# Performance work log

Hardware: AMD Instinct MI355X
Metric: run time of the kernel (lower is better)

## Reference

```python
import jax, jax.numpy as jnp
import numpy as np

BS, D, C, L_MAP, N_LAYERS, IMG = 8, 512, 128, 8, 9, 64


def _leaky(x):
    return jnp.where(x >= 0, x, 0.2 * x)


def _conv2d_mod(x, style, weight):
    # x: [bs, C, H, W], style: [bs, C], weight: [Cout, Cin, 3, 3]
    # modulate along input-channel dim, demodulate per (sample, out-channel)
    mw = weight[None] * style[:, None, :, None, None]          # [bs, Cout, Cin, 3, 3]
    rstd = jax.lax.rsqrt(jnp.sum(mw * mw, axis=(2, 3, 4), keepdims=True) + 1e-8)
    dw = mw * rstd                                             # demodulated per-sample weights

    def per_sample(xi, wi):
        return jax.lax.conv_general_dilated(
            xi[None], wi, window_strides=(1, 1), padding='SAME',
            dimension_numbers=('NCHW', 'OIHW', 'NCHW'))[0]

    return jax.vmap(per_sample)(x, dw)                         # [bs, C, H, W]


def _upsample2x(x):
    b, c, h, w = x.shape
    return jax.image.resize(x, (b, c, 2 * h, 2 * w), method='bilinear')


def setup_inputs():
    key = jax.random.key(0)
    ks = jax.random.split(key, 10)
    # kaiming fan_in gain for leaky_relu(a=0) per nn.init in Conv2dMod
    conv_std = float(np.sqrt(2.0 / (C * 9)))
    return {
        'latent_z': jax.random.normal(ks[0], (BS, D), jnp.float32),
        'noise': jax.random.normal(ks[1], (N_LAYERS, BS, IMG * IMG), jnp.float32),
        'map_w': jax.random.normal(ks[2], (L_MAP, D, D), jnp.float32) / np.sqrt(D),
        'map_b': jnp.zeros((L_MAP, D), jnp.float32),
        'A_w': jax.random.normal(ks[3], (N_LAYERS, D, C), jnp.float32) / np.sqrt(D),
        'A_b': jax.random.normal(ks[4], (N_LAYERS, C), jnp.float32) * 0.02 + 1.0,
        'B_w': jax.random.normal(ks[5], (N_LAYERS, C), jnp.float32),
        'B_b': jax.random.normal(ks[6], (N_LAYERS, C), jnp.float32) * 0.02,
        'conv_w': jax.random.normal(ks[7], (N_LAYERS, C, C, 3, 3), jnp.float32) * conv_std,
        'rgb_w': jax.random.normal(ks[8], (3, C, 3, 3), jnp.float32) / np.sqrt(C * 9),
        'rgb_b': jnp.zeros((3,), jnp.float32),
    }


def reference(latent_z, noise, map_w, map_b, A_w, A_b, B_w, B_b, conv_w, rgb_w, rgb_b):
    # ---- Mapping: PixelNorm + n_map_layers FC+LeakyReLU ----
    w = latent_z * jax.lax.rsqrt(jnp.mean(latent_z * latent_z, axis=1, keepdims=True) + 1e-8)
    for i in range(L_MAP):
        w = _leaky(w @ map_w[i] + map_b[i])                    # [bs, D] (same w for every style layer)

    # ---- Synthesis ----
    x = jnp.zeros((BS, C, 4, 4), latent_z.dtype)
    for i in range(N_LAYERS):
        if i % 2 == 1:
            x = _upsample2x(x)
        b, c, h, wd = x.shape
        ns = h * wd
        style = w @ A_w[i] + A_b[i]                            # [bs, C]
        # B: Linear(1, C) on per-pixel noise scalar -> per-channel noise map
        nmap = noise[i][:, :ns, None] * B_w[i][None, None, :] + B_b[i]  # [bs, ns, C]
        nmap = jnp.transpose(nmap, (0, 2, 1)).reshape(b, C, h, wd)
        x = _leaky(_conv2d_mod(x, style, conv_w[i]) + nmap)

    # ---- to RGB ----
    rgb = jax.lax.conv_general_dilated(
        x, rgb_w, window_strides=(1, 1), padding='SAME',
        dimension_numbers=('NCHW', 'OIHW', 'NCHW')) + rgb_b[None, :, None, None]
    return rgb
```

## Files before the change

### kernel.cpp

```cpp
#include <hip/hip_runtime.h>
#include <hip/hip_bf16.h>

#define BS 8
#define D 512
#define CCH 128
#define LMAP 8
#define NLAYERS 9

typedef short short8 __attribute__((ext_vector_type(8)));
typedef short short4v __attribute__((ext_vector_type(4)));
typedef float f32x4 __attribute__((ext_vector_type(4)));

__device__ short g_bufA[(size_t)BS * 4096 * CCH];
__device__ short g_bufB[(size_t)BS * 4096 * CCH];
__device__ float g_w[2][BS * D];
__device__ float g_style_all[NLAYERS * BS * CCH];
__device__ float g_rstd_all[NLAYERS * BS * CCH];
__device__ short g_wpack[(size_t)NLAYERS * 9 * 4 * 8 * 64 * 8];
__device__ short g_rgbpack[9 * 4 * 64 * 8];

__device__ __forceinline__ float leaky(float v) { return v >= 0.f ? v : 0.2f * v; }
__device__ __forceinline__ short f2b(float f) {
    __hip_bfloat16 h = __float2bfloat16(f);
    return *reinterpret_cast<short*>(&h);
}
__device__ __forceinline__ float b2f(short s) {
    return __uint_as_float(((unsigned int)(unsigned short)s) << 16);
}
__device__ __forceinline__ int swz(int col) { return ((col ^ (col >> 3)) & 7) << 3; }

__device__ __forceinline__ void uptaps(int o, int Win, int& i0, int& i1, float& w0, float& w1)
{
    int m = o >> 1;
    if ((o & 1) == 0) { i0 = m - 1; i1 = m; w0 = 0.25f; w1 = 0.75f; if (i0 < 0) { i0 = 0; w0 = 0.f; w1 = 1.f; } }
    else              { i0 = m; i1 = m + 1; w0 = 0.75f; w1 = 0.25f; if (i1 >= Win) { i1 = Win - 1; w0 = 1.f; w1 = 0.f; } }
}

__global__ __launch_bounds__(256) void wprep_kernel(const float* __restrict__ convw)
{
    int idx = blockIdx.x * 256 + threadIdx.x;
    if (idx >= NLAYERS * 9 * 4 * 8 * 64) return;
    int lane = idx & 63;
    int cogrp = (idx >> 6) & 7;
    int chunk = (idx >> 9) & 3;
    int t = idx >> 11;
    int layer = t / 9, tap = t - layer * 9;
    int co = cogrp * 16 + (lane & 15);
    int ci0 = chunk * 32 + (lane >> 4) * 8;
    short8 v;
#pragma unroll
    for (int j = 0; j < 8; ++j)
        v[j] = f2b(convw[(((size_t)layer * CCH + co) * CCH + ci0 + j) * 9 + tap]);
    *reinterpret_cast<short8*>(&g_wpack[(size_t)idx * 8]) = v;
}

__global__ void rgbprep_kernel(const float* __restrict__ rgbw)
{
    int idx = blockIdx.x * 256 + threadIdx.x;
    if (idx >= 9 * 4 * 64) return;
    int lane = idx & 63;
    int chunk = (idx >> 6) & 3;
    int tap = idx >> 8;
    int co = lane & 15;
    int ci0 = chunk * 32 + (lane >> 4) * 8;
    short8 v;
#pragma unroll
    for (int j = 0; j < 8; ++j)
        v[j] = (co < 3) ? f2b(rgbw[((size_t)(co * CCH) + ci0 + j) * 9 + tap]) : (short)0;
    *reinterpret_cast<short8*>(&g_rgbpack[(size_t)idx * 8]) = v;
}

__global__ __launch_bounds__(256) void map_fc_kernel(
    int srcSel, int useZ, const float* __restrict__ z,
    const float* __restrict__ W, const float* __restrict__ bias)
{
    float* wout = g_w[srcSel ^ 1];
    int b = blockIdx.y;
    int jb = blockIdx.x * 64;
    int tid = threadIdx.x;
    int jl = tid & 63, kp = tid >> 6;
    __shared__ float xin[D];
    __shared__ float part[4][64];
    __shared__ float wred[4];
    if (useZ) {
        xin[tid] = z[b * D + tid];
        xin[tid + 256] = z[b * D + tid + 256];
    } else {
        const float* win = g_w[srcSel];
        xin[tid] = win[b * D + tid];
        xin[tid + 256] = win[b * D + tid + 256];
    }
    __syncthreads();
    if (useZ) {
        float p = xin[tid] * xin[tid] + xin[tid + 256] * xin[tid + 256];
#pragma unroll
        for (int off = 32; off > 0; off >>= 1) p += __shfl_down(p, off, 64);
        if ((tid & 63) == 0) wred[tid >> 6] = p;
        __syncthreads();
        float ss = wred[0] + wred[1] + wred[2] + wred[3];
        float r = rsqrtf(ss * (1.f / 512.f) + 1e-8f);
        xin[tid] *= r; xin[tid + 256] *= r;
        __syncthreads();
    }
    const float* Wp = W + jb + jl;
    const int k0 = kp * 128;
    float a0 = 0.f, a1 = 0.f, a2 = 0.f, a3 = 0.f, a4 = 0.f, a5 = 0.f, a6 = 0.f, a7 = 0.f;
    for (int k = k0; k < k0 + 128; k += 8) {
        a0 += xin[k + 0] * Wp[(size_t)(k + 0) * D];
        a1 += xin[k + 1] * Wp[(size_t)(k + 1) * D];
        a2 += xin[k + 2] * Wp[(size_t)(k + 2) * D];
        a3 += xin[k + 3] * Wp[(size_t)(k + 3) * D];
        a4 += xin[k + 4] * Wp[(size_t)(k + 4) * D];
        a5 += xin[k + 5] * Wp[(size_t)(k + 5) * D];
        a6 += xin[k + 6] * Wp[(size_t)(k + 6) * D];
        a7 += xin[k + 7] * Wp[(size_t)(k + 7) * D];
    }
    part[kp][jl] = ((a0 + a1) + (a2 + a3)) + ((a4 + a5) + (a6 + a7));
    __syncthreads();
    if (tid < 64) {
        float s = part[0][tid] + part[1][tid] + part[2][tid] + part[3][tid] + bias[jb + tid];
        wout[b * D + jb + tid] = leaky(s);
    }
}

__global__ __launch_bounds__(256) void style_rstd_kernel(
    const float* __restrict__ Aw, const float* __restrict__ Ab,
    const float* __restrict__ convw)
{
    int l = blockIdx.x + 1;
    int b = blockIdx.y;
    int tid = threadIdx.x;
    __shared__ float ws_[D];
    __shared__ float part[2][CCH];
    __shared__ float st[CCH];
    ws_[tid] = g_w[0][b * D + tid];
    ws_[tid + 256] = g_w[0][b * D + tid + 256];
    __syncthreads();
    {
        int c = tid & 127, kh = tid >> 7;
        const float* Ap = Aw + (size_t)l * D * CCH + c;
        const int k0 = kh * 256;
        float a0 = 0.f, a1 = 0.f, a2 = 0.f, a3 = 0.f, a4 = 0.f, a5 = 0.f, a6 = 0.f, a7 = 0.f;
        for (int k = k0; k < k0 + 256; k += 8) {
            a0 += ws_[k + 0] * Ap[(size_t)(k + 0) * CCH];
            a1 += ws_[k + 1] * Ap[(size_t)(k + 1) * CCH];
            a2 += ws_[k + 2] * Ap[(size_t)(k + 2) * CCH];
            a3 += ws_[k + 3] * Ap[(size_t)(k + 3) * CCH];
            a4 += ws_[k + 4] * Ap[(size_t)(k + 4) * CCH];
            a5 += ws_[k + 5] * Ap[(size_t)(k + 5) * CCH];
            a6 += ws_[k + 6] * Ap[(size_t)(k + 6) * CCH];
            a7 += ws_[k + 7] * Ap[(size_t)(k + 7) * CCH];
        }
        part[kh][c] = ((a0 + a1) + (a2 + a3)) + ((a4 + a5) + (a6 + a7));
    }
    __syncthreads();
    if (tid < CCH) {
        float s = part[0][tid] + part[1][tid] + Ab[l * CCH + tid];
        st[tid] = s;
        g_style_all[((size_t)l * BS + b) * CCH + tid] = s;
    }
    __syncthreads();
    int colid = tid >> 4, kpart = tid & 15;
    for (int co8 = 0; co8 < 8; ++co8) {
        int cout = co8 * 16 + colid;
        const float* wp = convw + ((size_t)(l * CCH + cout) * CCH + kpart * 8) * 9;
        float wf[72];
#pragma unroll
        for (int q = 0; q < 18; ++q) {
            float4 t = *reinterpret_cast<const float4*>(wp + q * 4);
            wf[q * 4 + 0] = t.x; wf[q * 4 + 1] = t.y; wf[q * 4 + 2] = t.z; wf[q * 4 + 3] = t.w;
        }
        float s = 0.f;
#pragma unroll
        for (int ci = 0; ci < 8; ++ci) {
            float sv = st[kpart * 8 + ci];
#pragma unroll
            for (int k = 0; k < 9; ++k) { float m = wf[ci * 9 + k] * sv; s += m * m; }
        }
#pragma unroll
        for (int off = 8; off > 0; off >>= 1) s += __shfl_down(s, off, 16);
        if (kpart == 0) g_rstd_all[((size_t)l * BS + b) * CCH + cout] = rsqrtf(s + 1e-8f);
    }
}

template<int LW, int UPM>
__global__ __launch_bounds__(256) void conv_mfma_kernel(
    int srcSel, int layer, int layerNext,
    const float* __restrict__ noise,
    const float* __restrict__ Bw, const float* __restrict__ Bb,
    const float* __restrict__ noise0,
    const float* __restrict__ Bw0, const float* __restrict__ Bb0)
{
    constexpr int W = 1 << LW;
    constexpr int R = 64 >> LW;
    constexpr int SW = W + 2;
    constexpr int ROWS = R + 2;
    constexpr int NS = W * W;
    constexpr int WIN = W / 2;

    const short* xin = srcSel ? g_bufB : g_bufA;
    short* xout = srcSel ? g_bufA : g_bufB;

    const int b = blockIdx.y;
    const int pixBase = blockIdx.x * 64;
    const int rowBase = pixBase >> LW;
    const int tid = threadIdx.x;
    const int lane = tid & 63;
    const int wave = tid >> 6;
    const int wpx = wave & 1;
    const int wco = wave >> 1;

    __shared__ short xs[ROWS * SW * CCH];
    __shared__ float style_s[CCH];
    constexpr int SMSZ = (UPM == 2) ? 16 * CCH : 1;
    __shared__ short sm[SMSZ];

    if (tid < CCH)
        style_s[tid] = layerNext ? g_style_all[((size_t)layerNext * BS + b) * CCH + tid] : 1.f;

    if (UPM == 2) {
        for (int u = tid; u < 16 * CCH; u += 256) {
            int c = u & 127;
            int pp = u >> 7;
            float v = leaky(noise0[b * 4096 + pp] * Bw0[c] + Bb0[c])
                      * g_style_all[((size_t)1 * BS + b) * CCH + c];
            sm[u] = f2b(v);
        }
        __syncthreads();
    }

    {
        const short* src = xin + (size_t)b * NS * CCH;
        const short* srcH = xin + (size_t)b * WIN * WIN * CCH;
        constexpr int UN = ROWS * SW * 16;
        for (int u = tid; u < UN; u += 256) {
            int ck = u & 15;
            int rem = u >> 4;
            int col = rem % SW;
            int rr = rem / SW;
            int gy = rowBase + rr - 1, gx = col - 1;
            short8 v = {0, 0, 0, 0, 0, 0, 0, 0};
            if (gy >= 0 && gy < W && gx >= 0 && gx < W) {
                if (UPM == 0) {
                    v = *reinterpret_cast<const short8*>(&src[((size_t)gy * W + gx) * CCH + ck * 8]);
                } else {
                    int y0, y1, x0, x1; float wy0, wy1, wx0, wx1;
                    uptaps(gy, WIN, y0, y1, wy0, wy1);
                    uptaps(gx, WIN, x0, x1, wx0, wx1);
                    const short* sp = (UPM == 2) ? sm : srcH;
                    short8 a00 = *reinterpret_cast<const short8*>(&sp[((size_t)y0 * WIN + x0) * CCH + ck * 8]);
                    short8 a01 = *reinterpret_cast<const short8*>(&sp[((size_t)y0 * WIN + x1) * CCH + ck * 8]);
                    short8 a10 = *reinterpret_cast<const short8*>(&sp[((size_t)y1 * WIN + x0) * CCH + ck * 8]);
                    short8 a11 = *reinterpret_cast<const short8*>(&sp[((size_t)y1 * WIN + x1) * CCH + ck * 8]);
                    float w00 = wy0 * wx0, w01 = wy0 * wx1, w10 = wy1 * wx0, w11 = wy1 * wx1;
#pragma unroll
                    for (int j = 0; j < 8; ++j)
                        v[j] = f2b(w00 * b2f(a00[j]) + w01 * b2f(a01[j])
                                 + w10 * b2f(a10[j]) + w11 * b2f(a11[j]));
                }
            }
            *reinterpret_cast<short8*>(&xs[(((rr * SW + col) * CCH) + ck * 8) ^ swz(col)]) = v;
        }
    }
    __syncthreads();

    int rL[2], cL[2];
#pragma unroll
    for (int pf = 0; pf < 2; ++pf) {
        int pl = (wpx * 2 + pf) * 16 + (lane & 15);
        cL[pf] = pl & (W - 1);
        rL[pf] = pl >> LW;
    }
    const int grpoff = (lane >> 4) * 8;

    f32x4 acc[2][4] = {};
    const short* wl = g_wpack + ((size_t)layer * 9 * 4 * 8 * 64
                                 + (size_t)(wco * 4) * 64 + lane) * 8;

    short8 wc0 = *reinterpret_cast<const short8*>(wl);
    short8 wc1 = *reinterpret_cast<const short8*>(wl + 512);
    short8 wc2 = *reinterpret_cast<const short8*>(wl + 1024);
    short8 wc3 = *reinterpret_cast<const short8*>(wl + 1536);
#pragma unroll
    for (int k = 0; k < 36; ++k) {
        short8 wn0 = wc0, wn1 = wc1, wn2 = wc2, wn3 = wc3;
        if (k + 1 < 36) {
            const short* wk = wl + (size_t)(k + 1) * 4096;
            wn0 = *reinterpret_cast<const short8*>(wk);
            wn1 = *reinterpret_cast<const short8*>(wk + 512);
            wn2 = *reinterpret_cast<const short8*>(wk + 1024);
            wn3 = *reinterpret_cast<const short8*>(wk + 1536);
        }
        const int tap = k >> 2, ch = k & 3;
        const int ky = tap / 3, kx = tap - ky * 3;
#pragma unroll
        for (int pf = 0; pf < 2; ++pf) {
            int col = cL[pf] + kx;
            int idx = (((rL[pf] + ky) * SW + col) * CCH + (ch << 5) + grpoff) ^ swz(col);
            short8 xf = *reinterpret_cast<const short8*>(&xs[idx]);
            acc[pf][0] = __builtin_amdgcn_mfma_f32_16x16x32_bf16(wc0, xf, acc[pf][0], 0, 0, 0);
            acc[pf][1] = __builtin_amdgcn_mfma_f32_16x16x32_bf16(wc1, xf, acc[pf][1], 0, 0, 0);
            acc[pf][2] = __builtin_amdgcn_mfma_f32_16x16x32_bf16(wc2, xf, acc[pf][2], 0, 0, 0);
            acc[pf][3] = __builtin_amdgcn_mfma_f32_16x16x32_bf16(wc3, xf, acc[pf][3], 0, 0, 0);
        }
        wc0 = wn0; wc1 = wn1; wc2 = wn2; wc3 = wn3;
    }

    float nz[2];
#pragma unroll
    for (int pf = 0; pf < 2; ++pf)
        nz[pf] = noise[b * 4096 + pixBase + (wpx * 2 + pf) * 16 + (lane & 15)];
#pragma unroll
    for (int cf = 0; cf < 4; ++cf) {
        const int coB = (wco * 4 + cf) * 16 + (lane >> 4) * 4;
        float rs[4], bw[4], bb[4], sn[4];
#pragma unroll
        for (int r = 0; r < 4; ++r) {
            rs[r] = g_rstd_all[((size_t)layer * BS + b) * CCH + coB + r];
            bw[r] = Bw[coB + r];
            bb[r] = Bb[coB + r];
            sn[r] = style_s[coB + r];
        }
#pragma unroll
        for (int pf = 0; pf < 2; ++pf) {
            int px = pixBase + (wpx * 2 + pf) * 16 + (lane & 15);
            short4v o;
#pragma unroll
            for (int r = 0; r < 4; ++r) {
                float v = leaky(acc[pf][cf][r] * rs[r] + nz[pf] * bw[r] + bb[r]) * sn[r];
                o[r] = f2b(v);
            }
            *reinterpret_cast<short4v*>(&xout[((size_t)b * NS + px) * CCH + coB]) = o;
        }
    }
}

__global__ __launch_bounds__(256) void rgb_mfma_kernel(
    int srcSel, const float* __restrict__ rgbb, float* __restrict__ out)
{
    constexpr int W = 64, SW = 66, ROWS = 3, NS = 4096;
    const short* xin = srcSel ? g_bufB : g_bufA;

    const int b = blockIdx.y;
    const int pixBase = blockIdx.x * 64;
    const int rowBase = pixBase >> 6;
    const int tid = threadIdx.x;
    const int lane = tid & 63;
    const int wave = tid >> 6;

    __shared__ short xs[ROWS * SW * CCH];

    {
        const short* src = xin + (size_t)b * NS * CCH;
        constexpr int UN = ROWS * SW * 16;
        for (int u = tid; u < UN; u += 256) {
            int ck = u & 15;
            int rem = u >> 4;
            int col = rem % SW;
            int rr = rem / SW;
            int gy = rowBase + rr - 1, gx = col - 1;
            short8 v = {0, 0, 0, 0, 0, 0, 0, 0};
            if (gy >= 0 && gy < W && gx >= 0 && gx < W)
                v = *reinterpret_cast<const short8*>(&src[((size_t)gy * W + gx) * CCH + ck * 8]);
            *reinterpret_cast<short8*>(&xs[(((rr * SW + col) * CCH) + ck * 8) ^ swz(col)]) = v;
        }
    }
    __syncthreads();

    const int grpoff = (lane >> 4) * 8;
    const int cl = lane & 15;
    f32x4 acc[4] = {};
#pragma unroll
    for (int tap = 0; tap < 9; ++tap) {
        const int ky = tap / 3, kx = tap - ky * 3;
        short8 wf = *reinterpret_cast<const short8*>(
            &g_rgbpack[((size_t)(tap * 4 + wave) * 64 + lane) * 8]);
#pragma unroll
        for (int pf = 0; pf < 4; ++pf) {
            int col = cl + pf * 16 + kx;
            int idx = ((ky * SW + col) * CCH + (wave << 5) + grpoff) ^ swz(col);
            short8 xf = *reinterpret_cast<const short8*>(&xs[idx]);
            acc[pf] = __builtin_amdgcn_mfma_f32_16x16x32_bf16(wf, xf, acc[pf], 0, 0, 0);
        }
    }
    __syncthreads();
    float* red = reinterpret_cast<float*>(xs);
    if (wave > 0) {
#pragma unroll
        for (int pf = 0; pf < 4; ++pf)
#pragma unroll
            for (int r = 0; r < 4; ++r)
                red[(((wave - 1) * 4 + pf) * 64 + lane) * 4 + r] = acc[pf][r];
    }
    __syncthreads();
    if (wave == 0 && (lane >> 4) == 0) {
#pragma unroll
        for (int pf = 0; pf < 4; ++pf) {
            int px = pixBase + pf * 16 + cl;
#pragma unroll
            for (int r = 0; r < 3; ++r) {
                float s = acc[pf][r];
#pragma unroll
                for (int wv = 0; wv < 3; ++wv)
                    s += red[((wv * 4 + pf) * 64 + lane) * 4 + r];
                out[(size_t)(b * 3 + r) * NS + px] = s + rgbb[r];
            }
        }
    }
}

extern "C" void kernel_launch(void* const* d_in, const int* in_sizes, int n_in,
                              void* d_out, int out_size, void* d_ws, size_t ws_size,
                              hipStream_t stream)
{
    const float* latent = (const float*)d_in[0];
    const float* noise  = (const float*)d_in[1];
    const float* map_w  = (const float*)d_in[2];
    const float* map_b  = (const float*)d_in[3];
    const float* A_w    = (const float*)d_in[4];
    const float* A_b    = (const float*)d_in[5];
    const float* B_w    = (const float*)d_in[6];
    const float* B_b    = (const float*)d_in[7];
    const float* conv_w = (const float*)d_in[8];
    const float* rgb_w  = (const float*)d_in[9];
    const float* rgb_b  = (const float*)d_in[10];
    float* out = (float*)d_out;
    (void)d_ws; (void)ws_size;

    wprep_kernel<<<(NLAYERS * 9 * 4 * 8 * 64 + 255) / 256, 256, 0, stream>>>(conv_w);
    rgbprep_kernel<<<(9 * 4 * 64 + 255) / 256, 256, 0, stream>>>(rgb_w);

    int wsel = 0;
    for (int i = 0; i < LMAP; ++i) {
        map_fc_kernel<<<dim3(8, BS), 256, 0, stream>>>(
            wsel, i == 0 ? 1 : 0, latent, map_w + (size_t)i * D * D, map_b + i * D);
        wsel ^= 1;
    }

    style_rstd_kernel<<<dim3(8, BS), 256, 0, stream>>>(A_w, A_b, conv_w);

    int cur = 1;
    int Hc = 4;
    for (int i = 1; i < NLAYERS; ++i) {
        if (i & 1) Hc *= 2;
        int ns = Hc * Hc;
        int lnext = (i < 8) ? (i + 1) : 0;
        dim3 grid(ns / 64, BS);
        const float* nz = noise + (size_t)i * BS * 4096;
        switch (i) {
            case 1: conv_mfma_kernel<3, 2><<<grid, 256, 0, stream>>>(cur, i, lnext, nz, B_w + i * CCH, B_b + i * CCH, noise, B_w, B_b); break;
            case 2: conv_mfma_kernel<3, 0><<<grid, 256, 0, stream>>>(cur, i, lnext, nz, B_w + i * CCH, B_b + i * CCH, noise, B_w, B_b); break;
            case 3: conv_mfma_kernel<4, 1><<<grid, 256, 0, stream>>>(cur, i, lnext, nz, B_w + i * CCH, B_b + i * CCH, noise, B_w, B_b); break;
            case 4: conv_mfma_kernel<4, 0><<<grid, 256, 0, stream>>>(cur, i, lnext, nz, B_w + i * CCH, B_b + i * CCH, noise, B_w, B_b); break;
            case 5: conv_mfma_kernel<5, 1><<<grid, 256, 0, stream>>>(cur, i, lnext, nz, B_w + i * CCH, B_b + i * CCH, noise, B_w, B_b); break;
            case 6: conv_mfma_kernel<5, 0><<<grid, 256, 0, stream>>>(cur, i, lnext, nz, B_w + i * CCH, B_b + i * CCH, noise, B_w, B_b); break;
            case 7: conv_mfma_kernel<6, 1><<<grid, 256, 0, stream>>>(cur, i, lnext, nz, B_w + i * CCH, B_b + i * CCH, noise, B_w, B_b); break;
            case 8: conv_mfma_kernel<6, 0><<<grid, 256, 0, stream>>>(cur, i, lnext, nz, B_w + i * CCH, B_b + i * CCH, noise, B_w, B_b); break;
        }
        cur ^= 1;
    }

    rgb_mfma_kernel<<<dim3(64, BS), 256, 0, stream>>>(cur, rgb_b, out);
}
```

Baseline: 229.3 us.

## Fuse prep kernels, precompute weight sum-of-squares, fuse 8x8 conv layer pair

Merges the weight-pack and rgb-pack prep kernels into one launch. That launch also precomputes per-(cout,cin) sums of squared 3x3 weights, so the demodulation rstd becomes a cheap style-squared dot product. Layers 1 and 2 at 8x8 run in a single per-sample kernel that keeps the intermediate activation in shared memory, which removes one launch and a global round trip. The map FC loop is widened to 16 accumulators. The fused conv pair launches only 8 blocks, so its GPU utilisation is low.

```diff
diff --git a/kernel.cpp b/kernel.cpp
--- a/kernel.cpp
+++ b/kernel.cpp
@@ -16,6 +16,7 @@
 __device__ float g_w[2][BS * D];
 __device__ float g_style_all[NLAYERS * BS * CCH];
 __device__ float g_rstd_all[NLAYERS * BS * CCH];
+__device__ float g_s2[(size_t)NLAYERS * CCH * CCH];
 __device__ short g_wpack[(size_t)NLAYERS * 9 * 4 * 8 * 64 * 8];
 __device__ short g_rgbpack[9 * 4 * 64 * 8];
 
@@ -36,38 +37,46 @@
     else              { i0 = m; i1 = m + 1; w0 = 0.75f; w1 = 0.25f; if (i1 >= Win) { i1 = Win - 1; w0 = 1.f; w1 = 0.f; } }
 }
 
-__global__ __launch_bounds__(256) void wprep_kernel(const float* __restrict__ convw)
+#define WPN (NLAYERS * 9 * 4 * 8 * 64)
+#define RGBN (9 * 4 * 64)
+#define S2N (NLAYERS * CCH * CCH)
+__global__ __launch_bounds__(256) void prep_kernel(
+    const float* __restrict__ convw, const float* __restrict__ rgbw)
 {
     int idx = blockIdx.x * 256 + threadIdx.x;
-    if (idx >= NLAYERS * 9 * 4 * 8 * 64) return;
-    int lane = idx & 63;
-    int cogrp = (idx >> 6) & 7;
-    int chunk = (idx >> 9) & 3;
-    int t = idx >> 11;
-    int layer = t / 9, tap = t - layer * 9;
-    int co = cogrp * 16 + (lane & 15);
-    int ci0 = chunk * 32 + (lane >> 4) * 8;
-    short8 v;
-#pragma unroll
-    for (int j = 0; j < 8; ++j)
-        v[j] = f2b(convw[(((size_t)layer * CCH + co) * CCH + ci0 + j) * 9 + tap]);
-    *reinterpret_cast<short8*>(&g_wpack[(size_t)idx * 8]) = v;
-}
-
-__global__ void rgbprep_kernel(const float* __restrict__ rgbw)
-{
-    int idx = blockIdx.x * 256 + threadIdx.x;
-    if (idx >= 9 * 4 * 64) return;
-    int lane = idx & 63;
-    int chunk = (idx >> 6) & 3;
-    int tap = idx >> 8;
-    int co = lane & 15;
-    int ci0 = chunk * 32 + (lane >> 4) * 8;
-    short8 v;
-#pragma unroll
-    for (int j = 0; j < 8; ++j)
-        v[j] = (co < 3) ? f2b(rgbw[((size_t)(co * CCH) + ci0 + j) * 9 + tap]) : (short)0;
-    *reinterpret_cast<short8*>(&g_rgbpack[(size_t)idx * 8]) = v;
+    if (idx < WPN) {
+        int lane = idx & 63;
+        int cogrp = (idx >> 6) & 7;
+        int chunk = (idx >> 9) & 3;
+        int t = idx >> 11;
+        int layer = t / 9, tap = t - layer * 9;
+        int co = cogrp * 16 + (lane & 15);
+        int ci0 = chunk * 32 + (lane >> 4) * 8;
+        short8 v;
+#pragma unroll
+        for (int j = 0; j < 8; ++j)
+            v[j] = f2b(convw[(((size_t)layer * CCH + co) * CCH + ci0 + j) * 9 + tap]);
+        *reinterpret_cast<short8*>(&g_wpack[(size_t)idx * 8]) = v;
+    } else if (idx < WPN + RGBN) {
+        int u = idx - WPN;
+        int lane = u & 63;
+        int chunk = (u >> 6) & 3;
+        int tap = u >> 8;
+        int co = lane & 15;
+        int ci0 = chunk * 32 + (lane >> 4) * 8;
+        short8 v;
+#pragma unroll
+        for (int j = 0; j < 8; ++j)
+            v[j] = (co < 3) ? f2b(rgbw[((size_t)(co * CCH) + ci0 + j) * 9 + tap]) : (short)0;
+        *reinterpret_cast<short8*>(&g_rgbpack[(size_t)u * 8]) = v;
+    } else if (idx < WPN + RGBN + S2N) {
+        int u = idx - WPN - RGBN;
+        const float* wp = convw + (size_t)u * 9;
+        float s = 0.f;
+#pragma unroll
+        for (int t = 0; t < 9; ++t) { float m = wp[t]; s += m * m; }
+        g_s2[u] = s;
+    }
 }
 
 __global__ __launch_bounds__(256) void map_fc_kernel(
@@ -104,18 +113,18 @@
     }
     const float* Wp = W + jb + jl;
     const int k0 = kp * 128;
-    float a0 = 0.f, a1 = 0.f, a2 = 0.f, a3 = 0.f, a4 = 0.f, a5 = 0.f, a6 = 0.f, a7 = 0.f;
-    for (int k = k0; k < k0 + 128; k += 8) {
-        a0 += xin[k + 0] * Wp[(size_t)(k + 0) * D];
-        a1 += xin[k + 1] * Wp[(size_t)(k + 1) * D];
-        a2 += xin[k + 2] * Wp[(size_t)(k + 2) * D];
-        a3 += xin[k + 3] * Wp[(size_t)(k + 3) * D];
-        a4 += xin[k + 4] * Wp[(size_t)(k + 4) * D];
-        a5 += xin[k + 5] * Wp[(size_t)(k + 5) * D];
-        a6 += xin[k + 6] * Wp[(size_t)(k + 6) * D];
-        a7 += xin[k + 7] * Wp[(size_t)(k + 7) * D];
-    }
-    part[kp][jl] = ((a0 + a1) + (a2 + a3)) + ((a4 + a5) + (a6 + a7));
+    float a[16];
+#pragma unroll
+    for (int j = 0; j < 16; ++j) a[j] = 0.f;
+    for (int k = k0; k < k0 + 128; k += 16) {
+#pragma unroll
+        for (int j = 0; j < 16; ++j)
+            a[j] += xin[k + j] * Wp[(size_t)(k + j) * D];
+    }
+    float s8 = 0.f;
+#pragma unroll
+    for (int j = 0; j < 16; ++j) s8 += a[j];
+    part[kp][jl] = s8;
     __syncthreads();
     if (tid < 64) {
         float s = part[0][tid] + part[1][tid] + part[2][tid] + part[3][tid] + bias[jb + tid];
@@ -124,8 +133,7 @@
 }
 
 __global__ __launch_bounds__(256) void style_rstd_kernel(
-    const float* __restrict__ Aw, const float* __restrict__ Ab,
-    const float* __restrict__ convw)
+    const float* __restrict__ Aw, const float* __restrict__ Ab)
 {
     int l = blockIdx.x + 1;
     int b = blockIdx.y;
@@ -161,25 +169,209 @@
     }
     __syncthreads();
     int colid = tid >> 4, kpart = tid & 15;
+#pragma unroll
     for (int co8 = 0; co8 < 8; ++co8) {
         int cout = co8 * 16 + colid;
-        const float* wp = convw + ((size_t)(l * CCH + cout) * CCH + kpart * 8) * 9;
-        float wf[72];
-#pragma unroll
-        for (int q = 0; q < 18; ++q) {
-            float4 t = *reinterpret_cast<const float4*>(wp + q * 4);
-            wf[q * 4 + 0] = t.x; wf[q * 4 + 1] = t.y; wf[q * 4 + 2] = t.z; wf[q * 4 + 3] = t.w;
-        }
+        const float* sp = g_s2 + ((size_t)l * CCH + cout) * CCH + kpart * 8;
         float s = 0.f;
 #pragma unroll
-        for (int ci = 0; ci < 8; ++ci) {
-            float sv = st[kpart * 8 + ci];
-#pragma unroll
-            for (int k = 0; k < 9; ++k) { float m = wf[ci * 9 + k] * sv; s += m * m; }
-        }
+        for (int j = 0; j < 8; ++j) { float sv = st[kpart * 8 + j]; s += sv * sv * sp[j]; }
 #pragma unroll
         for (int off = 8; off > 0; off >>= 1) s += __shfl_down(s, off, 16);
         if (kpart == 0) g_rstd_all[((size_t)l * BS + b) * CCH + cout] = rsqrtf(s + 1e-8f);
+    }
+}
+
+__global__ __launch_bounds__(256) void conv8_pair_kernel(
+    const float* __restrict__ noise,
+    const float* __restrict__ Bw, const float* __restrict__ Bb)
+{
+    constexpr int W = 8, SW = 10, ROWS = 10, NS = 64, WIN = 4;
+    const int b = blockIdx.x;
+    const int tid = threadIdx.x;
+    const int lane = tid & 63;
+    const int wave = tid >> 6;
+    const int wpx = wave & 1;
+    const int wco = wave >> 1;
+
+    __shared__ short xs1[ROWS * SW * CCH];
+    __shared__ short xs2[ROWS * SW * CCH];
+    __shared__ short sm[16 * CCH];
+    __shared__ float style2_s[CCH], style3_s[CCH];
+
+    if (tid < CCH) {
+        style2_s[tid] = g_style_all[((size_t)2 * BS + b) * CCH + tid];
+        style3_s[tid] = g_style_all[((size_t)3 * BS + b) * CCH + tid];
+    }
+    for (int u = tid; u < 16 * CCH; u += 256) {
+        int c = u & 127;
+        int pp = u >> 7;
+        float v = leaky(noise[b * 4096 + pp] * Bw[c] + Bb[c])
+                  * g_style_all[((size_t)1 * BS + b) * CCH + c];
+        sm[u] = f2b(v);
+    }
+    for (int u = tid; u < ROWS * SW * 16; u += 256) {
+        int ck = u & 15;
+        int cell = u >> 4;
+        int col = cell % SW;
+        int rr = cell / SW;
+        if (rr >= 1 && rr <= 8 && col >= 1 && col <= 8) continue;
+        short8 z = {0, 0, 0, 0, 0, 0, 0, 0};
+        *reinterpret_cast<short8*>(&xs2[(((rr * SW + col) * CCH) + ck * 8) ^ swz(col)]) = z;
+    }
+    __syncthreads();
+
+    for (int u = tid; u < ROWS * SW * 16; u += 256) {
+        int ck = u & 15;
+        int rem = u >> 4;
+        int col = rem % SW;
+        int rr = rem / SW;
+        int gy = rr - 1, gx = col - 1;
+        short8 v = {0, 0, 0, 0, 0, 0, 0, 0};
+        if (gy >= 0 && gy < W && gx >= 0 && gx < W) {
+            int y0, y1, x0, x1; float wy0, wy1, wx0, wx1;
+            uptaps(gy, WIN, y0, y1, wy0, wy1);
+            uptaps(gx, WIN, x0, x1, wx0, wx1);
+            short8 a00 = *reinterpret_cast<const short8*>(&sm[((size_t)y0 * WIN + x0) * CCH + ck * 8]);
+            short8 a01 = *reinterpret_cast<const short8*>(&sm[((size_t)y0 * WIN + x1) * CCH + ck * 8]);
+            short8 a10 = *reinterpret_cast<const short8*>(&sm[((size_t)y1 * WIN + x0) * CCH + ck * 8]);
+            short8 a11 = *reinterpret_cast<const short8*>(&sm[((size_t)y1 * WIN + x1) * CCH + ck * 8]);
+            float w00 = wy0 * wx0, w01 = wy0 * wx1, w10 = wy1 * wx0, w11 = wy1 * wx1;
+#pragma unroll
+            for (int j = 0; j < 8; ++j)
+                v[j] = f2b(w00 * b2f(a00[j]) + w01 * b2f(a01[j])
+                         + w10 * b2f(a10[j]) + w11 * b2f(a11[j]));
+        }
+        *reinterpret_cast<short8*>(&xs1[(((rr * SW + col) * CCH) + ck * 8) ^ swz(col)]) = v;
+    }
+    __syncthreads();
+
+    int rL[2], cL[2];
+#pragma unroll
+    for (int pf = 0; pf < 2; ++pf) {
+        int pl = (wpx * 2 + pf) * 16 + (lane & 15);
+        cL[pf] = pl & (W - 1);
+        rL[pf] = pl >> 3;
+    }
+    const int grpoff = (lane >> 4) * 8;
+
+    {
+        f32x4 acc[2][4] = {};
+        const short* wl = g_wpack + ((size_t)1 * 9 * 4 * 8 * 64 + (size_t)(wco * 4) * 64 + lane) * 8;
+        short8 wc0 = *reinterpret_cast<const short8*>(wl);
+        short8 wc1 = *reinterpret_cast<const short8*>(wl + 512);
+        short8 wc2 = *reinterpret_cast<const short8*>(wl + 1024);
+        short8 wc3 = *reinterpret_cast<const short8*>(wl + 1536);
+#pragma unroll
+        for (int k = 0; k < 36; ++k) {
+            short8 wn0 = wc0, wn1 = wc1, wn2 = wc2, wn3 = wc3;
+            if (k + 1 < 36) {
+                const short* wk = wl + (size_t)(k + 1) * 4096;
+                wn0 = *reinterpret_cast<const short8*>(wk);
+                wn1 = *reinterpret_cast<const short8*>(wk + 512);
+                wn2 = *reinterpret_cast<const short8*>(wk + 1024);
+                wn3 = *reinterpret_cast<const short8*>(wk + 1536);
+            }
+            const int tap = k >> 2, ch = k & 3;
+            const int ky = tap / 3, kx = tap - ky * 3;
+#pragma unroll
+            for (int pf = 0; pf < 2; ++pf) {
+                int col = cL[pf] + kx;
+                int idx = (((rL[pf] + ky) * SW + col) * CCH + (ch << 5) + grpoff) ^ swz(col);
+                short8 xf = *reinterpret_cast<const short8*>(&xs1[idx]);
+                acc[pf][0] = __builtin_amdgcn_mfma_f32_16x16x32_bf16(wc0, xf, acc[pf][0], 0, 0, 0);
+                acc[pf][1] = __builtin_amdgcn_mfma_f32_16x16x32_bf16(wc1, xf, acc[pf][1], 0, 0, 0);
+                acc[pf][2] = __builtin_amdgcn_mfma_f32_16x16x32_bf16(wc2, xf, acc[pf][2], 0, 0, 0);
+                acc[pf][3] = __builtin_amdgcn_mfma_f32_16x16x32_bf16(wc3, xf, acc[pf][3], 0, 0, 0);
+            }
+            wc0 = wn0; wc1 = wn1; wc2 = wn2; wc3 = wn3;
+        }
+        float nz[2];
+#pragma unroll
+        for (int pf = 0; pf < 2; ++pf)
+            nz[pf] = noise[(size_t)BS * 4096 + b * 4096 + (wpx * 2 + pf) * 16 + (lane & 15)];
+#pragma unroll
+        for (int cf = 0; cf < 4; ++cf) {
+            const int coB = (wco * 4 + cf) * 16 + (lane >> 4) * 4;
+            float rs[4], bw[4], bb[4], sn[4];
+#pragma unroll
+            for (int r = 0; r < 4; ++r) {
+                rs[r] = g_rstd_all[((size_t)1 * BS + b) * CCH + coB + r];
+                bw[r] = Bw[1 * CCH + coB + r];
+                bb[r] = Bb[1 * CCH + coB + r];
+                sn[r] = style2_s[coB + r];
+            }
+#pragma unroll
+            for (int pf = 0; pf < 2; ++pf) {
+                int px = (wpx * 2 + pf) * 16 + (lane & 15);
+                int y = px >> 3, x = px & 7;
+                short4v o;
+#pragma unroll
+                for (int r = 0; r < 4; ++r)
+                    o[r] = f2b(leaky(acc[pf][cf][r] * rs[r] + nz[pf] * bw[r] + bb[r]) * sn[r]);
+                int col = x + 1;
+                *reinterpret_cast<short4v*>(&xs2[((((y + 1) * SW + col) * CCH) + coB) ^ swz(col)]) = o;
+            }
+        }
+    }
+    __syncthreads();
+
+    {
+        f32x4 acc[2][4] = {};
+        const short* wl = g_wpack + ((size_t)2 * 9 * 4 * 8 * 64 + (size_t)(wco * 4) * 64 + lane) * 8;
+        short8 wc0 = *reinterpret_cast<const short8*>(wl);
+        short8 wc1 = *reinterpret_cast<const short8*>(wl + 512);
+        short8 wc2 = *reinterpret_cast<const short8*>(wl + 1024);
+        short8 wc3 = *reinterpret_cast<const short8*>(wl + 1536);
+#pragma unroll
+        for (int k = 0; k < 36; ++k) {
+            short8 wn0 = wc0, wn1 = wc1, wn2 = wc2, wn3 = wc3;
+            if (k + 1 < 36) {
+                const short* wk = wl + (size_t)(k + 1) * 4096;
+                wn0 = *reinterpret_cast<const short8*>(wk);
+                wn1 = *reinterpret_cast<const short8*>(wk + 512);
+                wn2 = *reinterpret_cast<const short8*>(wk + 1024);
+                wn3 = *reinterpret_cast<const short8*>(wk + 1536);
+            }
+            const int tap = k >> 2, ch = k & 3;
+            const int ky = tap / 3, kx = tap - ky * 3;
+#pragma unroll
+            for (int pf = 0; pf < 2; ++pf) {
+                int col = cL[pf] + kx;
+                int idx = (((rL[pf] + ky) * SW + col) * CCH + (ch << 5) + grpoff) ^ swz(col);
+                short8 xf = *reinterpret_cast<const short8*>(&xs2[idx]);
+                acc[pf][0] = __builtin_amdgcn_mfma_f32_16x16x32_bf16(wc0, xf, acc[pf][0], 0, 0, 0);
+                acc[pf][1] = __builtin_amdgcn_mfma_f32_16x16x32_bf16(wc1, xf, acc[pf][1], 0, 0, 0);
+                acc[pf][2] = __builtin_amdgcn_mfma_f32_16x16x32_bf16(wc2, xf, acc[pf][2], 0, 0, 0);
+                acc[pf][3] = __builtin_amdgcn_mfma_f32_16x16x32_bf16(wc3, xf, acc[pf][3], 0, 0, 0);
+            }
+            wc0 = wn0; wc1 = wn1; wc2 = wn2; wc3 = wn3;
+        }
+        float nz[2];
+#pragma unroll
+        for (int pf = 0; pf < 2; ++pf)
+            nz[pf] = noise[(size_t)2 * BS * 4096 + b * 4096 + (wpx * 2 + pf) * 16 + (lane & 15)];
+#pragma unroll
+        for (int cf = 0; cf < 4; ++cf) {
+            const int coB = (wco * 4 + cf) * 16 + (lane >> 4) * 4;
+            float rs[4], bw[4], bb[4], sn[4];
+#pragma unroll
+            for (int r = 0; r < 4; ++r) {
+                rs[r] = g_rstd_all[((size_t)2 * BS + b) * CCH + coB + r];
+                bw[r] = Bw[2 * CCH + coB + r];
+                bb[r] = Bb[2 * CCH + coB + r];
+                sn[r] = style3_s[coB + r];
+            }
+#pragma unroll
+            for (int pf = 0; pf < 2; ++pf) {
+                int px = (wpx * 2 + pf) * 16 + (lane & 15);
+                short4v o;
+#pragma unroll
+                for (int r = 0; r < 4; ++r)
+                    o[r] = f2b(leaky(acc[pf][cf][r] * rs[r] + nz[pf] * bw[r] + bb[r]) * sn[r]);
+                *reinterpret_cast<short4v*>(&g_bufA[((size_t)b * NS + px) * CCH + coB]) = o;
+            }
+        }
     }
 }
 
@@ -187,9 +379,7 @@
 __global__ __launch_bounds__(256) void conv_mfma_kernel(
     int srcSel, int layer, int layerNext,
     const float* __restrict__ noise,
-    const float* __restrict__ Bw, const float* __restrict__ Bb,
-    const float* __restrict__ noise0,
-    const float* __restrict__ Bw0, const float* __restrict__ Bb0)
+    const float* __restrict__ Bw, const float* __restrict__ Bb)
 {
     constexpr int W = 1 << LW;
     constexpr int R = 64 >> LW;
@@ -212,22 +402,9 @@
 
     __shared__ short xs[ROWS * SW * CCH];
     __shared__ float style_s[CCH];
-    constexpr int SMSZ = (UPM == 2) ? 16 * CCH : 1;
-    __shared__ short sm[SMSZ];
 
     if (tid < CCH)
         style_s[tid] = layerNext ? g_style_all[((size_t)layerNext * BS + b) * CCH + tid] : 1.f;
-
-    if (UPM == 2) {
-        for (int u = tid; u < 16 * CCH; u += 256) {
-            int c = u & 127;
-            int pp = u >> 7;
-            float v = leaky(noise0[b * 4096 + pp] * Bw0[c] + Bb0[c])
-                      * g_style_all[((size_t)1 * BS + b) * CCH + c];
-            sm[u] = f2b(v);
-        }
-        __syncthreads();
-    }
 
     {
         const short* src = xin + (size_t)b * NS * CCH;
@@ -247,11 +424,10 @@
                     int y0, y1, x0, x1; float wy0, wy1, wx0, wx1;
                     uptaps(gy, WIN, y0, y1, wy0, wy1);
                     uptaps(gx, WIN, x0, x1, wx0, wx1);
-                    const short* sp = (UPM == 2) ? sm : srcH;
-                    short8 a00 = *reinterpret_cast<const short8*>(&sp[((size_t)y0 * WIN + x0) * CCH + ck * 8]);
-                    short8 a01 = *reinterpret_cast<const short8*>(&sp[((size_t)y0 * WIN + x1) * CCH + ck * 8]);
-                    short8 a10 = *reinterpret_cast<const short8*>(&sp[((size_t)y1 * WIN + x0) * CCH + ck * 8]);
-                    short8 a11 = *reinterpret_cast<const short8*>(&sp[((size_t)y1 * WIN + x1) * CCH + ck * 8]);
+                    short8 a00 = *reinterpret_cast<const short8*>(&srcH[((size_t)y0 * WIN + x0) * CCH + ck * 8]);
+                    short8 a01 = *reinterpret_cast<const short8*>(&srcH[((size_t)y0 * WIN + x1) * CCH + ck * 8]);
+                    short8 a10 = *reinterpret_cast<const short8*>(&srcH[((size_t)y1 * WIN + x0) * CCH + ck * 8]);
+                    short8 a11 = *reinterpret_cast<const short8*>(&srcH[((size_t)y1 * WIN + x1) * CCH + ck * 8]);
                     float w00 = wy0 * wx0, w01 = wy0 * wx1, w10 = wy1 * wx0, w11 = wy1 * wx1;
 #pragma unroll
                     for (int j = 0; j < 8; ++j)
@@ -427,8 +603,7 @@
     float* out = (float*)d_out;
     (void)d_ws; (void)ws_size;
 
-    wprep_kernel<<<(NLAYERS * 9 * 4 * 8 * 64 + 255) / 256, 256, 0, stream>>>(conv_w);
-    rgbprep_kernel<<<(9 * 4 * 64 + 255) / 256, 256, 0, stream>>>(rgb_w);
+    prep_kernel<<<(WPN + RGBN + S2N + 255) / 256, 256, 0, stream>>>(conv_w, rgb_w);
 
     int wsel = 0;
     for (int i = 0; i < LMAP; ++i) {
@@ -437,25 +612,25 @@
         wsel ^= 1;
     }
 
-    style_rstd_kernel<<<dim3(8, BS), 256, 0, stream>>>(A_w, A_b, conv_w);
-
-    int cur = 1;
-    int Hc = 4;
-    for (int i = 1; i < NLAYERS; ++i) {
+    style_rstd_kernel<<<dim3(8, BS), 256, 0, stream>>>(A_w, A_b);
+
+    conv8_pair_kernel<<<BS, 256, 0, stream>>>(noise, B_w, B_b);
+
+    int cur = 0;
+    int Hc = 8;
+    for (int i = 3; i < NLAYERS; ++i) {
         if (i & 1) Hc *= 2;
         int ns = Hc * Hc;
         int lnext = (i < 8) ? (i + 1) : 0;
         dim3 grid(ns / 64, BS);
         const float* nz = noise + (size_t)i * BS * 4096;
         switch (i) {
-            case 1: conv_mfma_kernel<3, 2><<<grid, 256, 0, stream>>>(cur, i, lnext, nz, B_w + i * CCH, B_b + i * CCH, noise, B_w, B_b); break;
-            case 2: conv_mfma_kernel<3, 0><<<grid, 256, 0, stream>>>(cur, i, lnext, nz, B_w + i * CCH, B_b + i * CCH, noise, B_w, B_b); break;
-            case 3: conv_mfma_kernel<4, 1><<<grid, 256, 0, stream>>>(cur, i, lnext, nz, B_w + i * CCH, B_b + i * CCH, noise, B_w, B_b); break;
-            case 4: conv_mfma_kernel<4, 0><<<grid, 256, 0, stream>>>(cur, i, lnext, nz, B_w + i * CCH, B_b + i * CCH, noise, B_w, B_b); break;
-            case 5: conv_mfma_kernel<5, 1><<<grid, 256, 0, stream>>>(cur, i, lnext, nz, B_w + i * CCH, B_b + i * CCH, noise, B_w, B_b); break;
-            case 6: conv_mfma_kernel<5, 0><<<grid, 256, 0, stream>>>(cur, i, lnext, nz, B_w + i * CCH, B_b + i * CCH, noise, B_w, B_b); break;
-            case 7: conv_mfma_kernel<6, 1><<<grid, 256, 0, stream>>>(cur, i, lnext, nz, B_w + i * CCH, B_b + i * CCH, noise, B_w, B_b); break;
-            case 8: conv_mfma_kernel<6, 0><<<grid, 256, 0, stream>>>(cur, i, lnext, nz, B_w + i * CCH, B_b + i * CCH, noise, B_w, B_b); break;
+            case 3: conv_mfma_kernel<4, 1><<<grid, 256, 0, stream>>>(cur, i, lnext, nz, B_w + i * CCH, B_b + i * CCH); break;
+            case 4: conv_mfma_kernel<4, 0><<<grid, 256, 0, stream>>>(cur, i, lnext, nz, B_w + i * CCH, B_b + i * CCH); break;
+            case 5: conv_mfma_kernel<5, 1><<<grid, 256, 0, stream>>>(cur, i, lnext, nz, B_w + i * CCH, B_b + i * CCH); break;
+            case 6: conv_mfma_kernel<5, 0><<<grid, 256, 0, stream>>>(cur, i, lnext, nz, B_w + i * CCH, B_b + i * CCH); break;
+            case 7: conv_mfma_kernel<6, 1><<<grid, 256, 0, stream>>>(cur, i, lnext, nz, B_w + i * CCH, B_b + i * CCH); break;
+            case 8: conv_mfma_kernel<6, 0><<<grid, 256, 0, stream>>>(cur, i, lnext, nz, B_w + i * CCH, B_b + i * CCH); break;
         }
         cur ^= 1;
     }
```

Measured after the change: 211.2 us. 7.9% less time.
